# Kernel optimization log

Hardware: AMD Instinct MI355X
Metric: run time of the kernel (lower is better)

## Reference

```python
import jax, jax.numpy as jnp
import numpy as np

RANK = 16
RATIO_1 = 0.01
RATIO_2 = 0.01
N_POWER_ITERS = 2  # randomized SVD power iterations (torch.svd_lowrank-style)


def _lowrank_V(A, rank, key):
    """Randomized low-rank right factor V (n, rank) of A (m, n), a la svd_lowrank."""
    m, n = A.shape
    omega = jax.random.normal(key, (n, rank), dtype=A.dtype)
    Q, _ = jnp.linalg.qr(A @ omega)              # (m, rank)
    for _ in range(N_POWER_ITERS):
        Z, _ = jnp.linalg.qr(A.T @ Q)            # (n, rank)
        Q, _ = jnp.linalg.qr(A @ Z)              # (m, rank)
    B = Q.T @ A                                  # (rank, n) small
    _, _, Vt = jnp.linalg.svd(B, full_matrices=False)
    return Vt.T                                  # (n, rank), orthonormal cols


def _get_statistics(x, ratio):
    # threshold such that ~ratio fraction of |x| entries are outliers
    return jnp.quantile(jnp.abs(x), 1.0 - ratio)


def _compress(x, thresh, rank, key):
    d = x.shape[-1]
    x2d = x.reshape(-1, d)                       # (M, D)
    outliers = jnp.where(jnp.abs(x2d) > thresh, x2d, jnp.zeros((), x2d.dtype))
    residual = x2d - outliers
    R = _lowrank_V(residual, rank, key)          # (D, rank)
    L = residual @ R                             # (M, rank)
    Rinv = R.T                                   # orthonormal cols -> pinv = R^T
    return outliers, L, R, Rinv


def reference(x1, x2):
    # Hadamard product (the module's returned value)
    result = x1 * x2
    # iteration == 0 path: compute statistics and run SVD compression
    out1 = _get_statistics(x1, RATIO_1)
    out2 = _get_statistics(x2, RATIO_2)
    k = jax.random.key(42)
    k1, k2 = jax.random.split(k)
    _, _, R1, Rinv1 = _compress(x1, out1, RANK, k1)
    _, _, R2, Rinv2 = _compress(x2, out2, RANK, k2)
    return (result, out1, R1, Rinv1, out2, R2, Rinv2)


def setup_inputs() -> dict:
    key = jax.random.key(0)
    k1, k2 = jax.random.split(key)
    x1 = jax.random.normal(k1, (4, 2048, 4096), dtype=jnp.float32)
    x2 = jax.random.normal(k2, (4, 2048, 4096), dtype=jnp.float32)
    return {"x1": x1, "x2": x2}
```

## Files before the change

### kernel.cpp

```cpp
#include <hip/hip_runtime.h>
#include <cstdint>
#include <cstddef>


#define DEV __device__ __forceinline__

typedef float nfloat4 __attribute__((ext_vector_type(4)));

constexpr long long NTOT = 33554432LL;
constexpr unsigned long long KSEL = 33218888ULL;

constexpr long long OUT_T1  = 33554432LL;
constexpr long long OUT_R1  = 33554433LL;
constexpr long long OUT_RI1 = 33619969LL;
constexpr long long OUT_T2  = 33685505LL;
constexpr long long OUT_R2  = 33685506LL;
constexpr long long OUT_RI2 = 33751042LL;

constexpr size_t OFF_SPEC   = 0;
constexpr size_t OFF_BPART  = 0;
constexpr size_t OFF_FB     = 4194304;
constexpr size_t OFF_CNT    = 6291456;
constexpr size_t ZERO_FLOATS= 6291472;
constexpr size_t OFF_CHIST  = 6291456;
constexpr size_t OFF_COARSE = 8388608;
constexpr size_t OFF_SEGS   = 8392704;
constexpr size_t OFF_SELR   = 8394752;
constexpr size_t OFF_TSEL   = 8394768;
constexpr size_t OFF_OMT    = 8394784;
constexpr size_t OFF_BIGY   = 8525856;
constexpr size_t OFF_BIGQ   = 8788000;
constexpr size_t OFF_ZT     = 9050144;
constexpr size_t OFF_QQR    = 9181216;
constexpr size_t OFF_TMAT   = 9312288;
constexpr size_t OFF_GRAMP  = 9443360;
constexpr size_t OFF_S      = 9476128;
constexpr size_t OFF_QTOP   = 9476640;
constexpr size_t OFF_RG     = 9477152;
constexpr size_t OFF_VTL    = 9477664;

#define TFR(a,b,r) { a += b; b = (b << r) | (b >> (32 - r)); b ^= a; }

DEV void d_threefry(uint32_t k0, uint32_t k1, uint32_t x0, uint32_t x1,
                    uint32_t& o0, uint32_t& o1){
  uint32_t ks2 = k0 ^ k1 ^ 0x1BD11BDAu;
  x0 += k0; x1 += k1;
  TFR(x0,x1,13) TFR(x0,x1,15) TFR(x0,x1,26) TFR(x0,x1,6)
  x0 += k1; x1 += ks2 + 1u;
  TFR(x0,x1,17) TFR(x0,x1,29) TFR(x0,x1,16) TFR(x0,x1,24)
  x0 += ks2; x1 += k0 + 2u;
  TFR(x0,x1,13) TFR(x0,x1,15) TFR(x0,x1,26) TFR(x0,x1,6)
  x0 += k0; x1 += k1 + 3u;
  TFR(x0,x1,17) TFR(x0,x1,29) TFR(x0,x1,16) TFR(x0,x1,24)
  x0 += k1; x1 += ks2 + 4u;
  TFR(x0,x1,13) TFR(x0,x1,15) TFR(x0,x1,26) TFR(x0,x1,6)
  x0 += ks2; x1 += k0 + 5u;
  o0 = x0; o1 = x1;
}

static void h_threefry(uint32_t k0, uint32_t k1, uint32_t x0, uint32_t x1,
                       uint32_t& o0, uint32_t& o1){
  uint32_t ks2 = k0 ^ k1 ^ 0x1BD11BDAu;
  x0 += k0; x1 += k1;
  TFR(x0,x1,13) TFR(x0,x1,15) TFR(x0,x1,26) TFR(x0,x1,6)
  x0 += k1; x1 += ks2 + 1u;
  TFR(x0,x1,17) TFR(x0,x1,29) TFR(x0,x1,16) TFR(x0,x1,24)
  x0 += ks2; x1 += k0 + 2u;
  TFR(x0,x1,13) TFR(x0,x1,15) TFR(x0,x1,26) TFR(x0,x1,6)
  x0 += k0; x1 += k1 + 3u;
  TFR(x0,x1,17) TFR(x0,x1,29) TFR(x0,x1,16) TFR(x0,x1,24)
  x0 += k1; x1 += ks2 + 4u;
  TFR(x0,x1,13) TFR(x0,x1,15) TFR(x0,x1,26) TFR(x0,x1,6)
  x0 += ks2; x1 += k0 + 5u;
  o0 = x0; o1 = x1;
}

DEV float erfinv_f32(float x){
  float w = -log1pf(-x*x);
  float p;
  if (w < 5.0f){
    w -= 2.5f;
    p = 2.81022636e-08f;
    p = fmaf(p, w, 3.43273939e-07f);
    p = fmaf(p, w, -3.5233877e-06f);
    p = fmaf(p, w, -4.39150654e-06f);
    p = fmaf(p, w, 0.00021858087f);
    p = fmaf(p, w, -0.00125372503f);
    p = fmaf(p, w, -0.00417768164f);
    p = fmaf(p, w, 0.246640727f);
    p = fmaf(p, w, 1.50140941f);
  } else {
    w = sqrtf(w) - 3.0f;
    p = -0.000200214257f;
    p = fmaf(p, w, 0.000100950558f);
    p = fmaf(p, w, 0.00134934322f);
    p = fmaf(p, w, -0.00367342844f);
    p = fmaf(p, w, 0.00573950773f);
    p = fmaf(p, w, -0.0076224613f);
    p = fmaf(p, w, 0.00943887047f);
    p = fmaf(p, w, 1.00167406f);
    p = fmaf(p, w, 2.83297682f);
  }
  return p * x;
}

DEV float lapy2f(float x, float y){
  float xa = fabsf(x), ya = fabsf(y);
  float w = fmaxf(xa, ya), z = fminf(xa, ya);
  if (z == 0.f) return w;
  float q = z / w;
  return w * sqrtf(1.f + q*q);
}

DEV void slartg_(float f, float g, float& c, float& s, float& r){
  if (g == 0.f){ c = 1.f; s = 0.f; r = f; }
  else if (f == 0.f){ c = 0.f; s = copysignf(1.f, g); r = fabsf(g); }
  else {
    float d = sqrtf(f*f + g*g);
    c = fabsf(f) / d;
    r = copysignf(d, f);
    s = g / r;
  }
}

DEV void slas2_(float f, float g, float h, float& ssmin, float& ssmax){
  float fa = fabsf(f), ga = fabsf(g), ha = fabsf(h);
  float fhmn = fminf(fa, ha), fhmx = fmaxf(fa, ha);
  if (fhmn == 0.f){
    ssmin = 0.f;
    if (fhmx == 0.f) ssmax = ga;
    else {
      float mx = fmaxf(fhmx, ga), mn = fminf(fhmx, ga);
      float q = mn/mx;
      ssmax = mx*sqrtf(1.f + q*q);
    }
  } else {
    if (ga < fhmx){
      float as_ = 1.f + fhmn/fhmx;
      float at_ = (fhmx - fhmn)/fhmx;
      float au = ga/fhmx; au = au*au;
      float cc = 2.f/(sqrtf(as_*as_ + au) + sqrtf(at_*at_ + au));
      ssmin = fhmn*cc; ssmax = fhmx/cc;
    } else {
      float au = fhmx/ga;
      if (au == 0.f){ ssmin = (fhmn*fhmx)/ga; ssmax = ga; }
      else {
        float as_ = 1.f + fhmn/fhmx;
        float at_ = (fhmx - fhmn)/fhmx;
        float q1 = as_*au, q2 = at_*au;
        float cc = 1.f/(sqrtf(1.f + q1*q1) + sqrtf(1.f + q2*q2));
        ssmin = (fhmn*cc)*au; ssmin = ssmin + ssmin;
        ssmax = ga/(cc + cc);
      }
    }
  }
}

DEV void slasv2_(float f, float g, float h, float& ssmin, float& ssmax,
                 float& snr, float& csr, float& snl, float& csl){
  const float eps = 5.9604645e-08f;
  float ft = f, fa = fabsf(f), ht = h, ha = fabsf(h);
  int pmax = 1;
  bool swp = (ha > fa);
  if (swp){ pmax = 3; float t; t=ft; ft=ht; ht=t; t=fa; fa=ha; ha=t; }
  float gt = g, ga = fabsf(g);
  float clt = 0.f, crt = 0.f, slt = 0.f, srt = 0.f;
  if (ga == 0.f){ ssmin = ha; ssmax = fa; clt = 1.f; crt = 1.f; slt = 0.f; srt = 0.f; }
  else {
    bool gasmal = true;
    if (ga > fa){
      pmax = 2;
      if ((fa/ga) < eps){
        gasmal = false;
        ssmax = ga;
        if (ha > 1.f) ssmin = fa/(ga/ha); else ssmin = (fa/ga)*ha;
        clt = 1.f; slt = ht/gt; srt = 1.f; crt = ft/gt;
      }
    }
    if (gasmal){
      float dd = fa - ha;
      float L = (dd == fa) ? 1.f : dd/fa;
      float Mv = gt/ft;
      float T = 2.f - L;
      float MM = Mv*Mv, TT = T*T;
      float Sv = sqrtf(TT + MM);
      float Rv = (L == 0.f) ? fabsf(Mv) : sqrtf(L*L + MM);
      float Av = 0.5f*(Sv + Rv);
      ssmin = ha/Av; ssmax = fa*Av;
      float Tv;
      if (MM == 0.f){
        if (L == 0.f) Tv = copysignf(2.f, ft)*copysignf(1.f, gt);
        else Tv = gt/copysignf(dd, ft) + Mv/T;
      } else {
        Tv = (Mv/(Sv + T) + Mv/(Rv + L))*(1.f + Av);
      }
      float Lv = sqrtf(Tv*Tv + 4.f);
      crt = 2.f/Lv; srt = Tv/Lv;
      clt = (crt + srt*Mv)/Av;
      slt = (ht/ft)*srt/Av;
    }
  }
  if (swp){ csl = srt; snl = crt; csr = slt; snr = clt; }
  else    { csl = clt; snl = slt; csr = crt; snr = srt; }
  float tsign = 1.f;
  if (pmax == 1) tsign = copysignf(1.f, csr)*copysignf(1.f, csl)*copysignf(1.f, f);
  if (pmax == 2) tsign = copysignf(1.f, snr)*copysignf(1.f, csl)*copysignf(1.f, g);
  if (pmax == 3) tsign = copysignf(1.f, snr)*copysignf(1.f, snl)*copysignf(1.f, h);
  ssmax = copysignf(ssmax, tsign);
  ssmin = copysignf(ssmin, tsign*copysignf(1.f, f)*copysignf(1.f, h));
}

__global__ __launch_bounds__(256) void k_had(const float* __restrict__ x1,
    const float* __restrict__ x2, float* __restrict__ out, float* __restrict__ ws){
  uint32_t* cnt = (uint32_t*)(ws + OFF_CNT);
  uint32_t* s1 = (uint32_t*)(ws + OFF_SPEC);
  uint32_t* s2 = s1 + 2097152;
  const float4* a4 = (const float4*)x1;
  const float4* b4 = (const float4*)x2;
  nfloat4* o4 = (nfloat4*)out;
  int cb1 = 0, c11 = 0, c21 = 0, cb2 = 0, c12 = 0, c22 = 0;
  long long n4 = NTOT/4;
  long long stride = (long long)gridDim.x * 256;
  for (long long i = (long long)blockIdx.x*256 + threadIdx.x; i < n4; i += stride){
    float4 a = a4[i], b = b4[i];
    nfloat4 o;
    o.x = a.x*b.x; o.y = a.y*b.y; o.z = a.z*b.z; o.w = a.w*b.w;
    __builtin_nontemporal_store(o, &o4[i]);
    uint32_t u, dd;
    u = __float_as_uint(a.x)&0x7fffffffu; cb1 += (u < 0x40100000u);
    dd = u - 0x40100000u;
    if (dd < 0x200000u){ atomicAdd(&s1[dd], 1u); if (dd < 0x100000u) c11++; else c21++; }
    u = __float_as_uint(a.y)&0x7fffffffu; cb1 += (u < 0x40100000u);
    dd = u - 0x40100000u;
    if (dd < 0x200000u){ atomicAdd(&s1[dd], 1u); if (dd < 0x100000u) c11++; else c21++; }
    u = __float_as_uint(a.z)&0x7fffffffu; cb1 += (u < 0x40100000u);
    dd = u - 0x40100000u;
    if (dd < 0x200000u){ atomicAdd(&s1[dd], 1u); if (dd < 0x100000u) c11++; else c21++; }
    u = __float_as_uint(a.w)&0x7fffffffu; cb1 += (u < 0x40100000u);
    dd = u - 0x40100000u;
    if (dd < 0x200000u){ atomicAdd(&s1[dd], 1u); if (dd < 0x100000u) c11++; else c21++; }
    u = __float_as_uint(b.x)&0x7fffffffu; cb2 += (u < 0x40100000u);
    dd = u - 0x40100000u;
    if (dd < 0x200000u){ atomicAdd(&s2[dd], 1u); if (dd < 0x100000u) c12++; else c22++; }
    u = __float_as_uint(b.y)&0x7fffffffu; cb2 += (u < 0x40100000u);
    dd = u - 0x40100000u;
    if (dd < 0x200000u){ atomicAdd(&s2[dd], 1u); if (dd < 0x100000u) c12++; else c22++; }
    u = __float_as_uint(b.z)&0x7fffffffu; cb2 += (u < 0x40100000u);
    dd = u - 0x40100000u;
    if (dd < 0x200000u){ atomicAdd(&s2[dd], 1u); if (dd < 0x100000u) c12++; else c22++; }
    u = __float_as_uint(b.w)&0x7fffffffu; cb2 += (u < 0x40100000u);
    dd = u - 0x40100000u;
    if (dd < 0x200000u){ atomicAdd(&s2[dd], 1u); if (dd < 0x100000u) c12++; else c22++; }
  }
  #pragma unroll
  for (int off = 32; off > 0; off >>= 1){
    cb1 += __shfl_xor(cb1, off, 64);
    c11 += __shfl_xor(c11, off, 64);
    c21 += __shfl_xor(c21, off, 64);
    cb2 += __shfl_xor(cb2, off, 64);
    c12 += __shfl_xor(c12, off, 64);
    c22 += __shfl_xor(c22, off, 64);
  }
  if ((threadIdx.x & 63) == 0){
    atomicAdd(&cnt[0], (uint32_t)cb1);
    atomicAdd(&cnt[1], (uint32_t)c11);
    atomicAdd(&cnt[2], (uint32_t)c21);
    atomicAdd(&cnt[3], (uint32_t)cb2);
    atomicAdd(&cnt[4], (uint32_t)c12);
    atomicAdd(&cnt[5], (uint32_t)c22);
  }
}

__global__ __launch_bounds__(64) void k_select(float* __restrict__ ws){
  if (threadIdx.x != 0) return;
  int ty = blockIdx.x;
  const uint32_t* cnt = (const uint32_t*)(ws + OFF_CNT) + ty*3;
  int* selr = (int*)(ws + OFF_SELR) + ty*4;
  unsigned long long cb = cnt[0], c1 = cnt[1], c2 = cnt[2], K = KSEL;
  if (K >= cb && K < cb + c1){
    selr[0] = 0x401; selr[1] = (int)(K - cb); selr[2] = 1;
  } else if (K >= cb + c1 && K < cb + c1 + c2){
    selr[0] = 0x402; selr[1] = (int)(K - cb - c1); selr[2] = 1;
  } else {
    selr[2] = 0;
  }
}

__global__ __launch_bounds__(256) void k_hist_fb(const float* __restrict__ x1,
    const float* __restrict__ x2, float* __restrict__ ws){
  const int* selr = (const int*)(ws + OFF_SELR);
  if (selr[2] && selr[4 + 2]) return;
  __shared__ uint32_t lh[2][4][2048];
  for (int i = threadIdx.x; i < 2*4*2048; i += 256) (&lh[0][0][0])[i] = 0u;
  __syncthreads();
  int rep = threadIdx.x & 3;
  const float4* a4 = (const float4*)x1;
  const float4* b4 = (const float4*)x2;
  long long n4 = NTOT/4;
  long long stride = (long long)gridDim.x * 256;
  for (long long i = (long long)blockIdx.x*256 + threadIdx.x; i < n4; i += stride){
    float4 a = a4[i], b = b4[i];
    uint32_t u;
    u = __float_as_uint(a.x)&0x7fffffffu; atomicAdd(&lh[0][rep][u>>20], 1u);
    u = __float_as_uint(a.y)&0x7fffffffu; atomicAdd(&lh[0][rep][u>>20], 1u);
    u = __float_as_uint(a.z)&0x7fffffffu; atomicAdd(&lh[0][rep][u>>20], 1u);
    u = __float_as_uint(a.w)&0x7fffffffu; atomicAdd(&lh[0][rep][u>>20], 1u);
    u = __float_as_uint(b.x)&0x7fffffffu; atomicAdd(&lh[1][rep][u>>20], 1u);
    u = __float_as_uint(b.y)&0x7fffffffu; atomicAdd(&lh[1][rep][u>>20], 1u);
    u = __float_as_uint(b.z)&0x7fffffffu; atomicAdd(&lh[1][rep][u>>20], 1u);
    u = __float_as_uint(b.w)&0x7fffffffu; atomicAdd(&lh[1][rep][u>>20], 1u);
  }
  __syncthreads();
  uint32_t* ch = (uint32_t*)(ws + OFF_CHIST);
  for (int i = threadIdx.x; i < 2048; i += 256){
    uint32_t c0 = lh[0][0][i] + lh[0][1][i] + lh[0][2][i] + lh[0][3][i];
    uint32_t c1 = lh[1][0][i] + lh[1][1][i] + lh[1][2][i] + lh[1][3][i];
    ch[((size_t)blockIdx.x*2 + 0)*2048 + i] = c0;
    ch[((size_t)blockIdx.x*2 + 1)*2048 + i] = c1;
  }
}

__global__ __launch_bounds__(256) void k_coarse_red(float* __restrict__ ws){
  int ty = blockIdx.y;
  if (((const int*)(ws + OFF_SELR))[ty*4 + 2]) return;
  const uint32_t* ch = (const uint32_t*)(ws + OFF_CHIST);
  uint32_t* h = (uint32_t*)(ws + OFF_COARSE) + ty*2048;
  int bin = blockIdx.x*128 + (threadIdx.x & 127);
  int half = threadIdx.x >> 7;
  uint32_t s = 0;
  for (int p = half*256; p < half*256 + 256; p++)
    s += ch[((size_t)p*2 + ty)*2048 + bin];
  __shared__ uint32_t sh[256];
  sh[threadIdx.x] = s;
  __syncthreads();
  if (threadIdx.x < 128) h[bin] = sh[threadIdx.x] + sh[threadIdx.x + 128];
}

__global__ __launch_bounds__(256) void k_coarse_scan(float* __restrict__ ws){
  int ty = blockIdx.x;
  int* selr = (int*)(ws + OFF_SELR) + ty*4;
  if (selr[2]) return;
  const uint32_t* h = (const uint32_t*)(ws + OFF_COARSE) + ty*2048;
  __shared__ unsigned long long ps[256];
  unsigned long long s = 0;
  for (int j = 0; j < 8; j++) s += h[threadIdx.x*8 + j];
  ps[threadIdx.x] = s;
  __syncthreads();
  if (threadIdx.x == 0){
    unsigned long long cum = 0, K = KSEL;
    int g = 0;
    for (; g < 256; g++){ if (cum + ps[g] > K) break; cum += ps[g]; }
    if (g > 255) g = 255;
    int bin = 2047;
    for (int j = 0; j < 8; j++){
      uint32_t c = h[g*8 + j];
      if (cum + c > K){ bin = g*8 + j; break; }
      cum += c;
    }
    selr[0] = bin;
    selr[1] = (int)(K - cum);
    selr[2] = 0;
  }
}

__global__ __launch_bounds__(256) void k_fine_fb(const float* __restrict__ x1,
    const float* __restrict__ x2, float* __restrict__ ws){
  int ty = blockIdx.y;
  const int* selr = (const int*)(ws + OFF_SELR) + ty*4;
  if (selr[2]) return;
  const float4* x4 = (const float4*)(ty ? x2 : x1);
  uint32_t bin = (uint32_t)selr[0];
  uint32_t* f = (uint32_t*)(ws + OFF_FB) + ((size_t)ty<<20);
  long long n4 = NTOT/4;
  long long stride = (long long)gridDim.x * 256;
  for (long long i = (long long)blockIdx.x*256 + threadIdx.x; i < n4; i += stride){
    float4 a = x4[i];
    uint32_t u;
    u = __float_as_uint(a.x)&0x7fffffffu; if ((u>>20)==bin) atomicAdd(&f[u&0xFFFFFu],1u);
    u = __float_as_uint(a.y)&0x7fffffffu; if ((u>>20)==bin) atomicAdd(&f[u&0xFFFFFu],1u);
    u = __float_as_uint(a.z)&0x7fffffffu; if ((u>>20)==bin) atomicAdd(&f[u&0xFFFFFu],1u);
    u = __float_as_uint(a.w)&0x7fffffffu; if ((u>>20)==bin) atomicAdd(&f[u&0xFFFFFu],1u);
  }
}

DEV const uint32_t* fine_base(const float* ws, int ty){
  const int* selr = (const int*)(ws + OFF_SELR) + ty*4;
  if (selr[2])
    return (const uint32_t*)(ws + OFF_SPEC) + ((size_t)ty<<21)
           + (((uint32_t)selr[0] - 0x401u) << 20);
  return (const uint32_t*)(ws + OFF_FB) + ((size_t)ty<<20);
}

__global__ __launch_bounds__(256) void k_seg_sum(float* __restrict__ ws){
  int ty = blockIdx.y;
  const uint32_t* f = fine_base(ws, ty);
  uint32_t* segs = (uint32_t*)(ws + OFF_SEGS) + ty*1024;
  uint32_t s = 0;
  int base = blockIdx.x*1024;
  for (int k = 0; k < 4; k++) s += f[base + k*256 + threadIdx.x];
  __shared__ uint32_t sh[256];
  sh[threadIdx.x] = s;
  __syncthreads();
  for (int off = 128; off > 0; off >>= 1){
    if (threadIdx.x < off) sh[threadIdx.x] += sh[threadIdx.x + off];
    __syncthreads();
  }
  if (threadIdx.x == 0) segs[blockIdx.x] = sh[0];
}

__global__ __launch_bounds__(256) void k_fine_scan2(float* __restrict__ ws, float* __restrict__ out){
  int ty = blockIdx.x;
  const uint32_t* f = fine_base(ws, ty);
  const uint32_t* segs = (const uint32_t*)(ws + OFF_SEGS) + ty*1024;
  const int* selr = (const int*)(ws + OFF_SELR) + ty*4;
  __shared__ uint32_t sh[1024];
  __shared__ uint32_t ps[256];
  __shared__ int gsel; __shared__ uint32_t csel;
  int t = threadIdx.x;
  uint32_t K = (uint32_t)selr[1];
  for (int k = 0; k < 4; k++) sh[k*256 + t] = segs[k*256 + t];
  __syncthreads();
  ps[t] = sh[4*t] + sh[4*t+1] + sh[4*t+2] + sh[4*t+3];
  __syncthreads();
  if (t == 0){
    uint32_t cum = 0; int q = 0;
    for (; q < 256; q++){ if (cum + ps[q] > K) break; cum += ps[q]; }
    if (q > 255) q = 255;
    int g = q*4;
    for (int j = 0; j < 4; j++){
      uint32_t c = sh[q*4 + j];
      if (cum + c > K){ g = q*4 + j; break; }
      cum += c;
      if (j == 3) g = q*4 + 3;
    }
    gsel = g; csel = cum;
  }
  __syncthreads();
  int g = gsel;
  for (int k = 0; k < 4; k++) sh[k*256 + t] = f[(size_t)g*1024 + k*256 + t];
  __syncthreads();
  ps[t] = sh[4*t] + sh[4*t+1] + sh[4*t+2] + sh[4*t+3];
  __syncthreads();
  if (t == 0){
    uint32_t cum = csel; int q = 0;
    for (; q < 256; q++){ if (cum + ps[q] > K) break; cum += ps[q]; }
    if (q > 255) q = 255;
    int j = q*4 + 3;
    for (int jj = 0; jj < 4; jj++){
      uint32_t c = sh[q*4 + jj];
      if (cum + c > K){ j = q*4 + jj; break; }
      cum += c;
    }
    uint32_t bits = (((uint32_t)selr[0])<<20) | (uint32_t)((g*1024 + j) & 0xFFFFF);
    float th = __uint_as_float(bits);
    ws[OFF_TSEL + ty] = th;
    out[ty ? OUT_T2 : OUT_T1] = th;
  }
}

__global__ __launch_bounds__(256) void k_omega(uint32_t a0, uint32_t a1,
    uint32_t b0, uint32_t b1, float* __restrict__ ws){
  int ty = blockIdx.y;
  uint32_t k0 = ty ? b0 : a0, k1 = ty ? b1 : a1;
  int i = blockIdx.x*256 + threadIdx.x;
  uint32_t o0, o1;
  d_threefry(k0, k1, 0u, (uint32_t)i, o0, o1);
  uint32_t bits = o0 ^ o1;
  float fr = __uint_as_float((bits >> 9) | 0x3f800000u) - 1.0f;
  const float lo = -0.99999994f;
  float u = fr * 2.0f + lo;
  u = fmaxf(lo, u);
  float v = 1.41421356237f * erfinv_f32(u);
  int row = i >> 4, col = i & 15;
  ws[OFF_OMT + (size_t)ty*65536 + (size_t)col*4096 + row] = v;
}

__global__ __launch_bounds__(256) void k_atype(const float* __restrict__ x1,
    const float* __restrict__ x2, float* __restrict__ ws, size_t wtOff){
  int ty = blockIdx.y;
  const float* x = ty ? x2 : x1;
  const float* wt = ws + wtOff + (size_t)ty*65536;
  float* Y = ws + OFF_BIGY + (size_t)ty*131072;
  float t = ws[OFF_TSEL + ty];
  int wave = threadIdx.x >> 6, lane = threadIdx.x & 63;
  __shared__ __align__(16) float wts[16][256];
  __shared__ float outs[16][16];
  float acc[4][16];
  #pragma unroll
  for (int r = 0; r < 4; r++)
    #pragma unroll
    for (int j = 0; j < 16; j++) acc[r][j] = 0.f;
  int rowbase = blockIdx.x*16 + wave*4;
  for (int c = 0; c < 4096; c += 256){
    __syncthreads();
    for (int idx = threadIdx.x; idx < 16*64; idx += 256){
      int j = idx >> 6, q = idx & 63;
      ((float4*)&wts[j][0])[q] = ((const float4*)(wt + (size_t)j*4096 + c))[q];
    }
    __syncthreads();
    float4 xv[4];
    #pragma unroll
    for (int rr = 0; rr < 4; rr++){
      int row = rowbase + rr;
      float4 a = ((const float4*)(x + (size_t)row*4096 + c))[lane];
      a.x = fabsf(a.x) > t ? 0.f : a.x;
      a.y = fabsf(a.y) > t ? 0.f : a.y;
      a.z = fabsf(a.z) > t ? 0.f : a.z;
      a.w = fabsf(a.w) > t ? 0.f : a.w;
      xv[rr] = a;
    }
    #pragma unroll
    for (int j = 0; j < 16; j++){
      float4 w4 = ((const float4*)&wts[j][0])[lane];
      #pragma unroll
      for (int rr = 0; rr < 4; rr++){
        acc[rr][j] = fmaf(xv[rr].x, w4.x, acc[rr][j]);
        acc[rr][j] = fmaf(xv[rr].y, w4.y, acc[rr][j]);
        acc[rr][j] = fmaf(xv[rr].z, w4.z, acc[rr][j]);
        acc[rr][j] = fmaf(xv[rr].w, w4.w, acc[rr][j]);
      }
    }
  }
  #pragma unroll
  for (int rr = 0; rr < 4; rr++)
    for (int j = 0; j < 16; j++){
      float v = acc[rr][j];
      for (int off = 32; off > 0; off >>= 1) v += __shfl_xor(v, off, 64);
      if (lane == 0) outs[wave*4 + rr][j] = v;
    }
  __syncthreads();
  int r = threadIdx.x >> 4, cc = threadIdx.x & 15;
  Y[(size_t)(blockIdx.x*16 + r)*16 + cc] = outs[r][cc];
}

__global__ __launch_bounds__(256) void k_gramP(float* __restrict__ ws, size_t mOff,
    size_t mStr){
  int ty = blockIdx.y;
  const float* M = ws + mOff + (size_t)ty*mStr;
  float* gp = ws + OFF_GRAMP + (size_t)(ty*64 + blockIdx.x)*256;
  __shared__ __align__(16) float buf[128][16];
  int t = threadIdx.x;
  for (int q = t; q < 512; q += 256)
    ((float4*)&buf[0][0])[q] = ((const float4*)(M + (size_t)blockIdx.x*2048))[q];
  __syncthreads();
  int i = t >> 4, j = t & 15;
  float s = 0.f;
  int rstart = (blockIdx.x == 0) ? 16 : 0;
  for (int r = rstart; r < 128; r++) s += buf[r][i]*buf[r][j];
  gp[t] = s;
}

__global__ __launch_bounds__(256) void k_btype(const float* __restrict__ x1,
    const float* __restrict__ x2, float* __restrict__ ws){
  int ty = blockIdx.y;
  const float* x = ty ? x2 : x1;
  const float* Q = ws + OFF_BIGQ + (size_t)ty*131072;
  float t = ws[OFF_TSEL + ty];
  int cb = blockIdx.x & 15;
  int rc = blockIdx.x >> 4;
  int c = cb*256 + threadIdx.x;
  int r0 = rc*512;
  __shared__ __align__(16) float Qs[64][16];
  float acc[16];
  #pragma unroll
  for (int j = 0; j < 16; j++) acc[j] = 0.f;
  for (int tile = 0; tile < 8; tile++){
    __syncthreads();
    ((float4*)&Qs[0][0])[threadIdx.x] =
        ((const float4*)(Q + (size_t)(r0 + tile*64)*16))[threadIdx.x];
    __syncthreads();
    const float* xp = x + (size_t)(r0 + tile*64)*4096 + c;
    #pragma unroll 4
    for (int rr = 0; rr < 64; rr++){
      float v = xp[(size_t)rr*4096];
      v = fabsf(v) > t ? 0.f : v;
      float4 qa = ((const float4*)&Qs[rr][0])[0];
      float4 qb = ((const float4*)&Qs[rr][0])[1];
      float4 qc = ((const float4*)&Qs[rr][0])[2];
      float4 qd = ((const float4*)&Qs[rr][0])[3];
      acc[ 0] = fmaf(v, qa.x, acc[ 0]);
      acc[ 1] = fmaf(v, qa.y, acc[ 1]);
      acc[ 2] = fmaf(v, qa.z, acc[ 2]);
      acc[ 3] = fmaf(v, qa.w, acc[ 3]);
      acc[ 4] = fmaf(v, qb.x, acc[ 4]);
      acc[ 5] = fmaf(v, qb.y, acc[ 5]);
      acc[ 6] = fmaf(v, qb.z, acc[ 6]);
      acc[ 7] = fmaf(v, qb.w, acc[ 7]);
      acc[ 8] = fmaf(v, qc.x, acc[ 8]);
      acc[ 9] = fmaf(v, qc.y, acc[ 9]);
      acc[10] = fmaf(v, qc.z, acc[10]);
      acc[11] = fmaf(v, qc.w, acc[11]);
      acc[12] = fmaf(v, qd.x, acc[12]);
      acc[13] = fmaf(v, qd.y, acc[13]);
      acc[14] = fmaf(v, qd.z, acc[14]);
      acc[15] = fmaf(v, qd.w, acc[15]);
    }
  }
  float* BP = ws + OFF_BPART + (((size_t)(ty*16 + rc))<<16) + (size_t)c*16;
  #pragma unroll
  for (int q = 0; q < 4; q++){
    float4 o; o.x = acc[q*4]; o.y = acc[q*4+1]; o.z = acc[q*4+2]; o.w = acc[q*4+3];
    ((float4*)BP)[q] = o;
  }
}

__global__ __launch_bounds__(256) void k_bredgram(float* __restrict__ ws){
  int ty = blockIdx.y;
  const float* BP = ws + OFF_BPART + (((size_t)ty*16)<<16);
  float* T = ws + OFF_TMAT + (size_t)ty*65536;
  float* gp = ws + OFF_GRAMP + (size_t)(ty*64 + blockIdx.x)*256;
  __shared__ float sh[64][16];
  int t = threadIdx.x;
  for (int k = 0; k < 4; k++){
    int e = blockIdx.x*1024 + k*256 + t;
    float s = 0.f;
    #pragma unroll
    for (int rc = 0; rc < 16; rc++) s += BP[((size_t)rc<<16) + e];
    T[e] = s;
    int le = k*256 + t;
    sh[le >> 4][le & 15] = s;
  }
  __syncthreads();
  int i = t >> 4, j = t & 15;
  float s = 0.f;
  int rstart = (blockIdx.x == 0) ? 16 : 0;
  for (int r = rstart; r < 64; r++) s += sh[r][i]*sh[r][j];
  gp[t] = s;
}

__global__ __launch_bounds__(64) void k_tiny(float* __restrict__ ws, size_t mOff,
    size_t mStr){
  int ty = blockIdx.x;
  const float* Mp = ws + mOff + (size_t)ty*mStr;
  float* sOut = ws + OFF_S + ty*256;
  float* qtOut = ws + OFF_QTOP + ty*256;
  float* rgOut = ws + OFF_RG + ty*256;
  __shared__ float G[16][16];
  __shared__ float Cld[32][16];
  __shared__ float bc[4];
  __shared__ float tau[16];
  int l = threadIdx.x;
  int j = l & 15;
  for (int e = l; e < 256; e += 64){
    const float* gp = ws + OFF_GRAMP + (size_t)ty*16384 + e;
    float s = 0.f;
    for (int p = 0; p < 64; p++) s += gp[(size_t)p*256];
    G[e>>4][e&15] = s;
  }
  for (int idx = l; idx < 256; idx += 64)
    Cld[idx>>4][idx&15] = Mp[idx];
  __syncthreads();
  for (int k = 0; k < 16; k++){
    float dk = sqrtf(G[k][k]);
    if (l == k) G[k][k] = dk;
    else if (l > k && l < 16) G[k][l] = G[k][l] / dk;
    __syncthreads();
    if (l > k && l < 16)
      for (int jj = l; jj < 16; jj++) G[l][jj] -= G[k][l]*G[k][jj];
    __syncthreads();
  }
  float Cc[32];
  #pragma unroll
  for (int r = 0; r < 32; r++){
    if (r < 16) Cc[r] = Cld[r][j];
    else Cc[r] = (j >= r - 16) ? G[r-16][j] : 0.f;
  }
  #pragma unroll
  for (int i = 0; i < 16; i++){
    if (l == i){
      float alpha = Cc[i];
      float ssum = 0.f;
      #pragma unroll
      for (int r = i+1; r < 32; r++) ssum += Cc[r]*Cc[r];
      float xn = sqrtf(ssum);
      float beta, tv, sc;
      if (xn == 0.f){ tv = 0.f; beta = alpha; sc = 1.f; }
      else {
        beta = -copysignf(lapy2f(alpha, xn), alpha);
        tv = (beta - alpha)/beta;
        sc = 1.f/(alpha - beta);
        #pragma unroll
        for (int r = i+1; r < 32; r++) Cc[r] *= sc;
      }
      Cc[i] = beta;
      bc[0] = beta; bc[1] = tv;
      tau[i] = tv;
      #pragma unroll
      for (int r = i; r < 32; r++) Cld[r][i] = Cc[r];
    }
    __syncthreads();
    float tv = bc[1];
    if (tv != 0.f && l < 16 && j > i){
      float w = Cc[i];
      #pragma unroll
      for (int r = i+1; r < 32; r++) w += Cld[r][i]*Cc[r];
      w *= tv;
      Cc[i] -= w;
      #pragma unroll
      for (int r = i+1; r < 32; r++) Cc[r] -= w*Cld[r][i];
    }
    __syncthreads();
  }
  float Qc[32];
  #pragma unroll
  for (int r = 0; r < 32; r++) Qc[r] = 0.f;
  #pragma unroll
  for (int i = 15; i >= 0; i--){
    float tv = tau[i];
    if (i < 15 && l < 16 && j > i){
      float w = Qc[i];
      #pragma unroll
      for (int r = i+1; r < 32; r++) w += Cld[r][i]*Qc[r];
      w *= tv;
      Qc[i] -= w;
      #pragma unroll
      for (int r = i+1; r < 32; r++) Qc[r] -= w*Cld[r][i];
    }
// ... 144 lines not shown
  for (int k = 0; k < 16; k++){
    D[k] = d_[k];
    E[k] = (k < 15) ? e_[k] : 0.f;
    vt[k] = (k == l) ? 1.f : 0.f;
  }
  auto getD = [&](int i)->float{ float r = D[0];
    #pragma unroll
    for (int k = 1; k < 16; k++) if (i == k) r = D[k];
    return r; };
  auto setD = [&](int i, float v){
    #pragma unroll
    for (int k = 0; k < 16; k++) if (i == k) D[k] = v; };
  auto getE = [&](int i)->float{ float r = E[0];
    #pragma unroll
    for (int k = 1; k < 16; k++) if (i == k) r = E[k];
    return r; };
  auto setE = [&](int i, float v){
    #pragma unroll
    for (int k = 0; k < 16; k++) if (i == k) E[k] = v; };
  auto getVt = [&](int i)->float{ float r = vt[0];
    #pragma unroll
    for (int k = 1; k < 16; k++) if (i == k) r = vt[k];
    return r; };
  auto setVt = [&](int i, float v){
    #pragma unroll
    for (int k = 0; k < 16; k++) if (i == k) vt[k] = v; };

  const float eps = 5.9604645e-08f;
  const float unfl = 1.17549435e-38f;
  const float tol = 10.f*eps;
  float sminoa = fabsf(D[0]);
  if (sminoa != 0.f){
    float mu = sminoa;
    #pragma unroll
    for (int i = 1; i < 16; i++){
      mu = fabsf(D[i])*(mu/(mu + fabsf(E[i-1])));
      sminoa = fminf(sminoa, mu);
    }
  }
  sminoa = sminoa / sqrtf((float)n);
  float thresh = fmaxf(tol*sminoa, (float)(6*n*n)*unfl);
  int maxit = 6*n*n;
  int iter = 0, oldll = -1, oldm = -1, mm = n, idir = 0;
  while (true){
    if (mm <= 1) break;
    if (iter > maxit) break;
    float smaxw = fabsf(getD(mm-1));
    int llv = 1; bool split = false;
    {
      bool done = false;
      #pragma unroll
      for (int c = 14; c >= 0; c--){
        if (c <= mm-2 && !done){
          if (fabsf(E[c]) <= thresh){ split = true; llv = c+1; done = true; }
          else smaxw = fmaxf(smaxw, fmaxf(fabsf(D[c]), fabsf(E[c])));
        }
      }
    }
    if (split){
      setE(llv-1, 0.f);
      if (llv == mm-1){ mm = mm - 1; continue; }
      llv = llv + 1;
    }
    if (llv == mm-1){
      float sigmn, sigmx, sinr, cosr, sinl, cosl;
      slasv2_(getD(mm-2), getE(mm-2), getD(mm-1), sigmn, sigmx, sinr, cosr, sinl, cosl);
      setD(mm-2, sigmx); setE(mm-2, 0.f); setD(mm-1, sigmn);
      float t1 = getVt(mm-2), t2 = getVt(mm-1);
      setVt(mm-2, cosr*t1 + sinr*t2);
      setVt(mm-1, cosr*t2 - sinr*t1);
      mm -= 2;
      continue;
    }
    if (llv > oldm || mm < oldll)
      idir = (fabsf(getD(llv-1)) >= fabsf(getD(mm-1))) ? 1 : 2;
    bool deflated = false;
    float sminl = 0.f;
    if (idir == 1){
      if (fabsf(getE(mm-2)) <= tol*fabsf(getD(mm-1))){ setE(mm-2, 0.f); continue; }
      float mu = fabsf(getD(llv-1)); sminl = mu;
      #pragma unroll
      for (int c = 0; c < 15; c++){
        if (c >= llv-1 && c <= mm-2 && !deflated){
          if (fabsf(E[c]) <= tol*mu){ E[c] = 0.f; deflated = true; }
          else {
            mu = fabsf(D[c+1])*(mu/(mu + fabsf(E[c])));
            sminl = fminf(sminl, mu);
          }
        }
      }
    } else {
      if (fabsf(getE(llv-1)) <= tol*fabsf(getD(llv-1))){ setE(llv-1, 0.f); continue; }
      float mu = fabsf(getD(mm-1)); sminl = mu;
      #pragma unroll
      for (int c = 14; c >= 0; c--){
        if (c >= llv-1 && c <= mm-2 && !deflated){
          if (fabsf(E[c]) <= tol*mu){ E[c] = 0.f; deflated = true; }
          else {
            mu = fabsf(D[c])*(mu/(mu + fabsf(E[c])));
            sminl = fminf(sminl, mu);
          }
        }
      }
    }
    if (deflated) continue;
    oldll = llv; oldm = mm;
    float shift = 0.f, rdum;
    if (!((float)n*tol*(sminl/smaxw) <= fmaxf(eps, 0.01f*tol))){
      float sll;
      if (idir == 1){ sll = fabsf(getD(llv-1)); slas2_(getD(mm-2), getE(mm-2), getD(mm-1), shift, rdum); }
      else          { sll = fabsf(getD(mm-1));  slas2_(getD(llv-1), getE(llv-1), getD(llv), shift, rdum); }
      if (sll > 0.f){ float q = shift/sll; if (q*q < eps) shift = 0.f; }
    }
    iter += mm - llv;
    if (shift == 0.f){
      if (idir == 1){
        float cs = 1.f, oldcs = 1.f, sn = 0.f, oldsn = 0.f, rr, dnew;
        #pragma unroll
        for (int i0 = 0; i0 < 15; i0++){
          if (i0 >= llv-1 && i0 <= mm-2){
            slartg_(D[i0]*cs, E[i0], cs, sn, rr);
            if (i0 > llv-1) E[i0-1 < 0 ? 0 : i0-1] = oldsn*rr;
            slartg_(oldcs*rr, D[i0+1]*sn, oldcs, oldsn, dnew);
            D[i0] = dnew;
            if (cs != 1.f || sn != 0.f){
              float t1 = vt[i0], t2 = vt[i0+1];
              vt[i0+1] = cs*t2 - sn*t1;
              vt[i0]   = sn*t2 + cs*t1;
            }
          }
        }
        float h = getD(mm-1)*cs;
        setD(mm-1, h*oldcs);
        float hv = h*oldsn;
        setE(mm-2, (fabsf(hv) <= thresh) ? 0.f : hv);
      } else {
        float cs = 1.f, oldcs = 1.f, sn = 0.f, oldsn = 0.f, rr, dnew;
        #pragma unroll
        for (int i0 = 15; i0 >= 1; i0--){
          if (i0 >= llv && i0 <= mm-1){
            slartg_(D[i0]*cs, E[i0-1], cs, sn, rr);
            if (i0 < mm-1) E[i0] = oldsn*rr;
            slartg_(oldcs*rr, D[i0-1]*sn, oldcs, oldsn, dnew);
            D[i0] = dnew;
            float cR = oldcs, sR = -oldsn;
            if (cR != 1.f || sR != 0.f){
              float t1 = vt[i0-1], t2 = vt[i0];
              vt[i0]   = cR*t2 - sR*t1;
              vt[i0-1] = sR*t2 + cR*t1;
            }
          }
        }
        float h = getD(llv-1)*cs;
        setD(llv-1, h*oldcs);
        float hv = h*oldsn;
        setE(llv-1, (fabsf(hv) <= thresh) ? 0.f : hv);
      }
    } else {
      if (idir == 1){
        float dl = getD(llv-1);
        float ff = (fabsf(dl) - shift)*(copysignf(1.f, dl) + shift/dl);
        float gg = getE(llv-1);
        float cosr, sinr, cosl, sinl, rr;
        #pragma unroll
        for (int i0 = 0; i0 < 15; i0++){
          if (i0 >= llv-1 && i0 <= mm-2){
            slartg_(ff, gg, cosr, sinr, rr);
            if (i0 > llv-1) E[i0-1 < 0 ? 0 : i0-1] = rr;
            float di = D[i0], ei = E[i0];
            ff = cosr*di + sinr*ei;
            E[i0] = cosr*ei - sinr*di;
            gg = sinr*D[i0+1];
            D[i0+1] = cosr*D[i0+1];
            slartg_(ff, gg, cosl, sinl, rr);
            D[i0] = rr;
            float ei2 = E[i0], dip = D[i0+1];
            ff = cosl*ei2 + sinl*dip;
            D[i0+1] = cosl*dip - sinl*ei2;
            if (i0 < mm-2){
              gg = sinl*E[i0+1];
              E[i0+1] = cosl*E[i0+1];
            }
            if (cosr != 1.f || sinr != 0.f){
              float t1 = vt[i0], t2 = vt[i0+1];
              vt[i0+1] = cosr*t2 - sinr*t1;
              vt[i0]   = sinr*t2 + cosr*t1;
            }
          }
        }
        setE(mm-2, (fabsf(ff) <= thresh) ? 0.f : ff);
      } else {
        float dm = getD(mm-1);
        float ff = (fabsf(dm) - shift)*(copysignf(1.f, dm) + shift/dm);
        float gg = getE(mm-2);
        float cosr, sinr, cosl, sinl, rr;
        #pragma unroll
        for (int i0 = 15; i0 >= 1; i0--){
          if (i0 >= llv && i0 <= mm-1){
            slartg_(ff, gg, cosr, sinr, rr);
            if (i0 < mm-1) E[i0] = rr;
            float di = D[i0], eim = E[i0-1];
            ff = cosr*di + sinr*eim;
            E[i0-1] = cosr*eim - sinr*di;
            gg = sinr*D[i0-1];
            D[i0-1] = cosr*D[i0-1];
            slartg_(ff, gg, cosl, sinl, rr);
            D[i0] = rr;
            float eim2 = E[i0-1], dim = D[i0-1];
            ff = cosl*eim2 + sinl*dim;
            D[i0-1] = cosl*dim - sinl*eim2;
            if (i0 > llv){
              gg = sinl*E[i0-2 < 0 ? 0 : i0-2];
              E[i0-2 < 0 ? 0 : i0-2] = cosl*E[i0-2 < 0 ? 0 : i0-2];
            }
            float cR = cosr, sR = -sinr;
            if (cR != 1.f || sR != 0.f){
              float t1 = vt[i0-1], t2 = vt[i0];
              vt[i0]   = cR*t2 - sR*t1;
              vt[i0-1] = sR*t2 + cR*t1;
            }
          }
        }
        setE(llv-1, (fabsf(ff) <= thresh) ? 0.f : ff);
      }
    }
  }
  #pragma unroll
  for (int k = 0; k < 16; k++){
    if (D[k] < 0.f){ D[k] = -D[k]; vt[k] = -vt[k]; }
  }
  #pragma unroll
  for (int i = 1; i <= 15; i++){
    int isub = 1; float smn = D[0];
    #pragma unroll
    for (int jj = 2; jj <= 16; jj++){
      if (jj <= 16 + 1 - i){
        if (D[jj-1] <= smn){ isub = jj; smn = D[jj-1]; }
      }
    }
    if (isub != 16 + 1 - i){
      setD(isub - 1, D[16 - i]);
      D[16 - i] = smn;
      float tmp = getVt(isub - 1);
      setVt(isub - 1, vt[16 - i]);
      vt[16 - i] = tmp;
    }
  }
  if (l < 16){
    #pragma unroll
    for (int r = 0; r < 16; r++) VTm[r][l] = vt[r];
  }
  __syncthreads();
  for (int i = n-2; i >= 0; i--){
    float tp = taup[i];
    if (tp != 0.f && l < 16){
      int r = l;
      float w = VTm[r][i+1];
      for (int c = i+2; c < n; c++) w += VTm[r][c]*A[i][c];
      w *= tp;
      VTm[r][i+1] -= w;
      for (int c = i+2; c < n; c++) VTm[r][c] -= w*A[i][c];
    }
    __syncthreads();
  }
  for (int idx = l; idx < 256; idx += 64) vtlOut[idx] = VTm[idx>>4][idx&15];
}

__global__ __launch_bounds__(256) void k_rout(float* __restrict__ ws, float* __restrict__ out){
  int ty = blockIdx.y;
  const float* Qq = ws + OFF_QQR + (size_t)ty*65536;
  const float* vtl = ws + OFF_VTL + ty*256;
  long long Roff  = ty ? OUT_R2  : OUT_R1;
  long long RIoff = ty ? OUT_RI2 : OUT_RI1;
  __shared__ float V[16][16];
  int t = threadIdx.x;
  V[t>>4][t&15] = vtl[t];
  __syncthreads();
  int row = blockIdx.x*256 + t;
  float mv[16];
  #pragma unroll
  for (int q = 0; q < 4; q++){
    float4 v = ((const float4*)(Qq + (size_t)row*16))[q];
    mv[q*4] = v.x; mv[q*4+1] = v.y; mv[q*4+2] = v.z; mv[q*4+3] = v.w;
  }
  #pragma unroll
  for (int j = 0; j < 16; j++){
    float s = 0.f;
    #pragma unroll
    for (int i = 0; i < 16; i++) s = fmaf(mv[i], V[j][i], s);
    out[Roff + (long long)row*16 + j] = s;
    out[RIoff + (long long)j*4096 + row] = s;
  }
}

extern "C" void kernel_launch(void* const* d_in, const int* in_sizes, int n_in,
                              void* d_out, int out_size, void* d_ws, size_t ws_size,
                              hipStream_t stream){
  const float* x1 = (const float*)d_in[0];
  const float* x2 = (const float*)d_in[1];
  float* out = (float*)d_out;
  float* ws = (float*)d_ws;
  (void)in_sizes; (void)n_in; (void)out_size; (void)ws_size;

  hipMemsetAsync(d_ws, 0, ZERO_FLOATS*sizeof(float), stream);

  k_had<<<dim3(1024), 256, 0, stream>>>(x1, x2, out, ws);
  k_select<<<dim3(2), 64, 0, stream>>>(ws);
  k_hist_fb<<<dim3(512), 256, 0, stream>>>(x1, x2, ws);
  k_coarse_red<<<dim3(16, 2), 256, 0, stream>>>(ws);
  k_coarse_scan<<<dim3(2), 256, 0, stream>>>(ws);
  k_fine_fb<<<dim3(1024, 2), 256, 0, stream>>>(x1, x2, ws);
  k_seg_sum<<<dim3(1024, 2), 256, 0, stream>>>(ws);
  k_fine_scan2<<<dim3(2), 256, 0, stream>>>(ws, out);

  uint32_t a0, a1, b0, b1;
  h_threefry(0u, 42u, 0u, 0u, a0, a1);
  h_threefry(0u, 42u, 0u, 1u, b0, b1);
  k_omega<<<dim3(256, 2), 256, 0, stream>>>(a0, a1, b0, b1, ws);

  k_atype<<<dim3(512, 2), 256, 0, stream>>>(x1, x2, ws, OFF_OMT);
  k_gramP<<<dim3(64, 2), 256, 0, stream>>>(ws, OFF_BIGY, 131072);
  k_tiny<<<dim3(2), 64, 0, stream>>>(ws, OFF_BIGY, 131072);
  k_applyq<<<dim3(32, 2), 256, 0, stream>>>(ws, OFF_BIGY, 131072, OFF_BIGQ, 131072, 8192, 1, 0);
  k_btype<<<dim3(256, 2), 256, 0, stream>>>(x1, x2, ws);
  k_bredgram<<<dim3(64, 2), 256, 0, stream>>>(ws);
  k_tiny<<<dim3(2), 64, 0, stream>>>(ws, OFF_TMAT, 65536);
  k_applyq<<<dim3(16, 2), 256, 0, stream>>>(ws, OFF_TMAT, 65536, OFF_ZT, 65536, 4096, 0, 1);
  k_atype<<<dim3(512, 2), 256, 0, stream>>>(x1, x2, ws, OFF_ZT);
  k_gramP<<<dim3(64, 2), 256, 0, stream>>>(ws, OFF_BIGY, 131072);
  k_tiny<<<dim3(2), 64, 0, stream>>>(ws, OFF_BIGY, 131072);
  k_applyq<<<dim3(32, 2), 256, 0, stream>>>(ws, OFF_BIGY, 131072, OFF_BIGQ, 131072, 8192, 1, 0);
  k_btype<<<dim3(256, 2), 256, 0, stream>>>(x1, x2, ws);
  k_bredgram<<<dim3(64, 2), 256, 0, stream>>>(ws);
  k_tiny<<<dim3(2), 64, 0, stream>>>(ws, OFF_TMAT, 65536);
  k_applyq<<<dim3(16, 2), 256, 0, stream>>>(ws, OFF_TMAT, 65536, OFF_ZT, 65536, 4096, 0, 1);
  k_atype<<<dim3(512, 2), 256, 0, stream>>>(x1, x2, ws, OFF_ZT);
  k_gramP<<<dim3(64, 2), 256, 0, stream>>>(ws, OFF_BIGY, 131072);
  k_tiny<<<dim3(2), 64, 0, stream>>>(ws, OFF_BIGY, 131072);
  k_applyq<<<dim3(32, 2), 256, 0, stream>>>(ws, OFF_BIGY, 131072, OFF_BIGQ, 131072, 8192, 1, 0);
  k_btype<<<dim3(256, 2), 256, 0, stream>>>(x1, x2, ws);
  k_bredgram<<<dim3(64, 2), 256, 0, stream>>>(ws);
  k_tiny<<<dim3(2), 64, 0, stream>>>(ws, OFF_TMAT, 65536);
  k_applyq<<<dim3(16, 2), 256, 0, stream>>>(ws, OFF_TMAT, 65536, OFF_QQR, 65536, 4096, 1, 0);

  k_chain<<<dim3(2), 64, 0, stream>>>(ws);
  k_rout<<<dim3(16, 2), 256, 0, stream>>>(ws, out);
}
```

Baseline: 1.854 ms.

## Replace global speculative fine histogram with per-block shared-memory two-level select

The Hadamard pass now builds a coarse 2048-bin histogram of the speculative window in shared memory and writes one partial per block, instead of doing global atomics into a 2M-entry speculative histogram. New kernels reduce the partials, select a coarse bin, rescan the input with shared-memory atomics to build a 1024-bin fine histogram, and pick the threshold. The memset shrinks because the large speculative region no longer needs zeroing. The cost is an extra full read of each input for the fine pass and 16MB of per-block partials to write and reduce.

Measured after the change: 1.705 ms. 1.09x faster.

```diff
diff --git a/kernel.cpp b/kernel.cpp
--- a/kernel.cpp
+++ b/kernel.cpp
@@ -9,6 +9,7 @@
 
 constexpr long long NTOT = 33554432LL;
 constexpr unsigned long long KSEL = 33218888ULL;
+constexpr uint32_t WLO = 0x40100000u;
 
 constexpr long long OUT_T1  = 33554432LL;
 constexpr long long OUT_R1  = 33554433LL;
@@ -17,11 +18,13 @@
 constexpr long long OUT_R2  = 33685506LL;
 constexpr long long OUT_RI2 = 33751042LL;
 
-constexpr size_t OFF_SPEC   = 0;
+constexpr size_t OFF_WPART  = 0;
 constexpr size_t OFF_BPART  = 0;
 constexpr size_t OFF_FB     = 4194304;
 constexpr size_t OFF_CNT    = 6291456;
-constexpr size_t ZERO_FLOATS= 6291472;
+constexpr size_t OFF_GF     = 6291472;
+constexpr size_t ZERO_BASE  = OFF_FB;
+constexpr size_t ZERO_FLOATS= 2099216;
 constexpr size_t OFF_CHIST  = 6291456;
 constexpr size_t OFF_COARSE = 8388608;
 constexpr size_t OFF_SEGS   = 8392704;
@@ -212,13 +215,14 @@
 
 __global__ __launch_bounds__(256) void k_had(const float* __restrict__ x1,
     const float* __restrict__ x2, float* __restrict__ out, float* __restrict__ ws){
+  __shared__ uint32_t wh[2][2048];
+  for (int i = threadIdx.x; i < 4096; i += 256) (&wh[0][0])[i] = 0u;
+  __syncthreads();
   uint32_t* cnt = (uint32_t*)(ws + OFF_CNT);
-  uint32_t* s1 = (uint32_t*)(ws + OFF_SPEC);
-  uint32_t* s2 = s1 + 2097152;
   const float4* a4 = (const float4*)x1;
   const float4* b4 = (const float4*)x2;
   nfloat4* o4 = (nfloat4*)out;
-  int cb1 = 0, c11 = 0, c21 = 0, cb2 = 0, c12 = 0, c22 = 0;
+  uint32_t cb1 = 0, cb2 = 0;
   long long n4 = NTOT/4;
   long long stride = (long long)gridDim.x * 256;
   for (long long i = (long long)blockIdx.x*256 + threadIdx.x; i < n4; i += stride){
@@ -227,62 +231,141 @@
     o.x = a.x*b.x; o.y = a.y*b.y; o.z = a.z*b.z; o.w = a.w*b.w;
     __builtin_nontemporal_store(o, &o4[i]);
     uint32_t u, dd;
-    u = __float_as_uint(a.x)&0x7fffffffu; cb1 += (u < 0x40100000u);
-    dd = u - 0x40100000u;
-    if (dd < 0x200000u){ atomicAdd(&s1[dd], 1u); if (dd < 0x100000u) c11++; else c21++; }
-    u = __float_as_uint(a.y)&0x7fffffffu; cb1 += (u < 0x40100000u);
-    dd = u - 0x40100000u;
-    if (dd < 0x200000u){ atomicAdd(&s1[dd], 1u); if (dd < 0x100000u) c11++; else c21++; }
-    u = __float_as_uint(a.z)&0x7fffffffu; cb1 += (u < 0x40100000u);
-    dd = u - 0x40100000u;
-    if (dd < 0x200000u){ atomicAdd(&s1[dd], 1u); if (dd < 0x100000u) c11++; else c21++; }
-    u = __float_as_uint(a.w)&0x7fffffffu; cb1 += (u < 0x40100000u);
-    dd = u - 0x40100000u;
-    if (dd < 0x200000u){ atomicAdd(&s1[dd], 1u); if (dd < 0x100000u) c11++; else c21++; }
-    u = __float_as_uint(b.x)&0x7fffffffu; cb2 += (u < 0x40100000u);
-    dd = u - 0x40100000u;
-    if (dd < 0x200000u){ atomicAdd(&s2[dd], 1u); if (dd < 0x100000u) c12++; else c22++; }
-    u = __float_as_uint(b.y)&0x7fffffffu; cb2 += (u < 0x40100000u);
-    dd = u - 0x40100000u;
-    if (dd < 0x200000u){ atomicAdd(&s2[dd], 1u); if (dd < 0x100000u) c12++; else c22++; }
-    u = __float_as_uint(b.z)&0x7fffffffu; cb2 += (u < 0x40100000u);
-    dd = u - 0x40100000u;
-    if (dd < 0x200000u){ atomicAdd(&s2[dd], 1u); if (dd < 0x100000u) c12++; else c22++; }
-    u = __float_as_uint(b.w)&0x7fffffffu; cb2 += (u < 0x40100000u);
-    dd = u - 0x40100000u;
-    if (dd < 0x200000u){ atomicAdd(&s2[dd], 1u); if (dd < 0x100000u) c12++; else c22++; }
-  }
+    u = __float_as_uint(a.x)&0x7fffffffu; cb1 += (u < WLO); dd = u - WLO;
+    if (dd < 0x200000u) atomicAdd(&wh[0][dd>>10], 1u);
+    u = __float_as_uint(a.y)&0x7fffffffu; cb1 += (u < WLO); dd = u - WLO;
+    if (dd < 0x200000u) atomicAdd(&wh[0][dd>>10], 1u);
+    u = __float_as_uint(a.z)&0x7fffffffu; cb1 += (u < WLO); dd = u - WLO;
+    if (dd < 0x200000u) atomicAdd(&wh[0][dd>>10], 1u);
+    u = __float_as_uint(a.w)&0x7fffffffu; cb1 += (u < WLO); dd = u - WLO;
+    if (dd < 0x200000u) atomicAdd(&wh[0][dd>>10], 1u);
+    u = __float_as_uint(b.x)&0x7fffffffu; cb2 += (u < WLO); dd = u - WLO;
+    if (dd < 0x200000u) atomicAdd(&wh[1][dd>>10], 1u);
+    u = __float_as_uint(b.y)&0x7fffffffu; cb2 += (u < WLO); dd = u - WLO;
+    if (dd < 0x200000u) atomicAdd(&wh[1][dd>>10], 1u);
+    u = __float_as_uint(b.z)&0x7fffffffu; cb2 += (u < WLO); dd = u - WLO;
+    if (dd < 0x200000u) atomicAdd(&wh[1][dd>>10], 1u);
+    u = __float_as_uint(b.w)&0x7fffffffu; cb2 += (u < WLO); dd = u - WLO;
+    if (dd < 0x200000u) atomicAdd(&wh[1][dd>>10], 1u);
+  }
+  __syncthreads();
+  uint32_t* wp = (uint32_t*)(ws + OFF_WPART) + (size_t)blockIdx.x*4096;
+  for (int i = threadIdx.x; i < 4096; i += 256) wp[i] = (&wh[0][0])[i];
   #pragma unroll
   for (int off = 32; off > 0; off >>= 1){
     cb1 += __shfl_xor(cb1, off, 64);
-    c11 += __shfl_xor(c11, off, 64);
-    c21 += __shfl_xor(c21, off, 64);
     cb2 += __shfl_xor(cb2, off, 64);
-    c12 += __shfl_xor(c12, off, 64);
-    c22 += __shfl_xor(c22, off, 64);
   }
   if ((threadIdx.x & 63) == 0){
-    atomicAdd(&cnt[0], (uint32_t)cb1);
-    atomicAdd(&cnt[1], (uint32_t)c11);
-    atomicAdd(&cnt[2], (uint32_t)c21);
-    atomicAdd(&cnt[3], (uint32_t)cb2);
-    atomicAdd(&cnt[4], (uint32_t)c12);
-    atomicAdd(&cnt[5], (uint32_t)c22);
-  }
-}
-
-__global__ __launch_bounds__(64) void k_select(float* __restrict__ ws){
-  if (threadIdx.x != 0) return;
+    atomicAdd(&cnt[0], cb1);
+    atomicAdd(&cnt[1], cb2);
+  }
+}
+
+__global__ __launch_bounds__(1024) void k_red(float* __restrict__ ws){
+  int ty = blockIdx.y;
+  const uint32_t* wp = (const uint32_t*)(ws + OFF_WPART);
+  uint32_t* H = (uint32_t*)(ws + OFF_COARSE) + ty*2048;
+  int t = threadIdx.x;
+  int bin = blockIdx.x*256 + (t & 255);
+  int pq = t >> 8;
+  uint32_t s = 0;
+  for (int p = pq*256; p < pq*256 + 256; p++)
+    s += wp[(size_t)p*4096 + (size_t)ty*2048 + bin];
+  __shared__ uint32_t sh[1024];
+  sh[t] = s;
+  __syncthreads();
+  if (t < 256) H[bin] = sh[t] + sh[t+256] + sh[t+512] + sh[t+768];
+}
+
+__global__ __launch_bounds__(256) void k_wselect(float* __restrict__ ws){
   int ty = blockIdx.x;
-  const uint32_t* cnt = (const uint32_t*)(ws + OFF_CNT) + ty*3;
+  const uint32_t* H = (const uint32_t*)(ws + OFF_COARSE) + ty*2048;
+  const uint32_t* cnt = (const uint32_t*)(ws + OFF_CNT);
   int* selr = (int*)(ws + OFF_SELR) + ty*4;
-  unsigned long long cb = cnt[0], c1 = cnt[1], c2 = cnt[2], K = KSEL;
-  if (K >= cb && K < cb + c1){
-    selr[0] = 0x401; selr[1] = (int)(K - cb); selr[2] = 1;
-  } else if (K >= cb + c1 && K < cb + c1 + c2){
-    selr[0] = 0x402; selr[1] = (int)(K - cb - c1); selr[2] = 1;
-  } else {
-    selr[2] = 0;
+  __shared__ unsigned long long ps[256];
+  unsigned long long s = 0;
+  for (int j = 0; j < 8; j++) s += H[threadIdx.x*8 + j];
+  ps[threadIdx.x] = s;
+  __syncthreads();
+  if (threadIdx.x == 0){
+    unsigned long long K = KSEL, cum = cnt[ty];
+    int valid = 0, sbin = 0, rank = 0;
+    if (K >= cum){
+      int g = 0;
+      for (; g < 256; g++){ if (cum + ps[g] > K) break; cum += ps[g]; }
+      if (g < 256){
+        for (int j = 0; j < 8; j++){
+          uint32_t c = H[g*8 + j];
+          if (cum + c > K){ sbin = g*8 + j; rank = (int)(K - cum); valid = 1; break; }
+          cum += c;
+        }
+      }
+    }
+    selr[0] = sbin; selr[1] = rank; selr[2] = valid;
+  }
+}
+
+__global__ __launch_bounds__(256) void k_fine(const float* __restrict__ x1,
+    const float* __restrict__ x2, float* __restrict__ ws){
+  int ty = blockIdx.y;
+  const int* selr = (const int*)(ws + OFF_SELR) + ty*4;
+  if (!selr[2]) return;
+  uint32_t g = (uint32_t)selr[0];
+  __shared__ uint32_t lh[1024];
+  for (int i = threadIdx.x; i < 1024; i += 256) lh[i] = 0u;
+  __syncthreads();
+  const float4* x4 = (const float4*)(ty ? x2 : x1);
+  long long n4 = NTOT/4;
+  long long stride = (long long)gridDim.x * 256;
+  for (long long i = (long long)blockIdx.x*256 + threadIdx.x; i < n4; i += stride){
+    float4 a = x4[i];
+    uint32_t dd;
+    dd = (__float_as_uint(a.x)&0x7fffffffu) - WLO;
+    if ((dd>>10) == g) atomicAdd(&lh[dd & 1023u], 1u);
+    dd = (__float_as_uint(a.y)&0x7fffffffu) - WLO;
+    if ((dd>>10) == g) atomicAdd(&lh[dd & 1023u], 1u);
+    dd = (__float_as_uint(a.z)&0x7fffffffu) - WLO;
+    if ((dd>>10) == g) atomicAdd(&lh[dd & 1023u], 1u);
+    dd = (__float_as_uint(a.w)&0x7fffffffu) - WLO;
+    if ((dd>>10) == g) atomicAdd(&lh[dd & 1023u], 1u);
+  }
+  __syncthreads();
+  uint32_t* gf = (uint32_t*)(ws + OFF_GF) + (size_t)ty*1024;
+  for (int i = threadIdx.x; i < 1024; i += 256){
+    uint32_t v = lh[i];
+    if (v) atomicAdd(&gf[i], v);
+  }
+}
+
+__global__ __launch_bounds__(256) void k_fine_sel(float* __restrict__ ws,
+    float* __restrict__ out){
+  int ty = blockIdx.x;
+  const int* selr = (const int*)(ws + OFF_SELR) + ty*4;
+  if (!selr[2]) return;
+  const uint32_t* gf = (const uint32_t*)(ws + OFF_GF) + (size_t)ty*1024;
+  __shared__ uint32_t sh[1024];
+  __shared__ uint32_t ps[256];
+  int t = threadIdx.x;
+  for (int k = 0; k < 4; k++) sh[k*256 + t] = gf[k*256 + t];
+  __syncthreads();
+  ps[t] = sh[4*t] + sh[4*t+1] + sh[4*t+2] + sh[4*t+3];
+  __syncthreads();
+  if (t == 0){
+    uint32_t K = (uint32_t)selr[1];
+    uint32_t cum = 0; int q = 0;
+    for (; q < 256; q++){ if (cum + ps[q] > K) break; cum += ps[q]; }
+    if (q > 255) q = 255;
+    int f = q*4 + 3;
+    for (int jj = 0; jj < 4; jj++){
+      uint32_t c = sh[q*4 + jj];
+      if (cum + c > K){ f = q*4 + jj; break; }
+      cum += c;
+    }
+    uint32_t bits = WLO + (((uint32_t)selr[0]) << 10) + (uint32_t)f;
+    float th = __uint_as_float(bits);
+    ws[OFF_TSEL + ty] = th;
+    out[ty ? OUT_T2 : OUT_T1] = th;
   }
 }
 
@@ -359,7 +442,6 @@
     }
     selr[0] = bin;
     selr[1] = (int)(K - cum);
-    selr[2] = 0;
   }
 }
 
@@ -383,17 +465,11 @@
   }
 }
 
-DEV const uint32_t* fine_base(const float* ws, int ty){
-  const int* selr = (const int*)(ws + OFF_SELR) + ty*4;
-  if (selr[2])
-    return (const uint32_t*)(ws + OFF_SPEC) + ((size_t)ty<<21)
-           + (((uint32_t)selr[0] - 0x401u) << 20);
-  return (const uint32_t*)(ws + OFF_FB) + ((size_t)ty<<20);
-}
-
 __global__ __launch_bounds__(256) void k_seg_sum(float* __restrict__ ws){
   int ty = blockIdx.y;
-  const uint32_t* f = fine_base(ws, ty);
+  const int* selr = (const int*)(ws + OFF_SELR) + ty*4;
+  if (selr[2]) return;
+  const uint32_t* f = (const uint32_t*)(ws + OFF_FB) + ((size_t)ty<<20);
   uint32_t* segs = (uint32_t*)(ws + OFF_SEGS) + ty*1024;
   uint32_t s = 0;
   int base = blockIdx.x*1024;
@@ -410,9 +486,10 @@
 
 __global__ __launch_bounds__(256) void k_fine_scan2(float* __restrict__ ws, float* __restrict__ out){
   int ty = blockIdx.x;
-  const uint32_t* f = fine_base(ws, ty);
+  const int* selr = (const int*)(ws + OFF_SELR) + ty*4;
+  if (selr[2]) return;
+  const uint32_t* f = (const uint32_t*)(ws + OFF_FB) + ((size_t)ty<<20);
   const uint32_t* segs = (const uint32_t*)(ws + OFF_SEGS) + ty*1024;
-  const int* selr = (const int*)(ws + OFF_SELR) + ty*4;
   __shared__ uint32_t sh[1024];
   __shared__ uint32_t ps[256];
   __shared__ int gsel; __shared__ uint32_t csel;
@@ -1163,10 +1240,13 @@
   float* ws = (float*)d_ws;
   (void)in_sizes; (void)n_in; (void)out_size; (void)ws_size;
 
-  hipMemsetAsync(d_ws, 0, ZERO_FLOATS*sizeof(float), stream);
+  hipMemsetAsync(ws + ZERO_BASE, 0, ZERO_FLOATS*sizeof(float), stream);
 
   k_had<<<dim3(1024), 256, 0, stream>>>(x1, x2, out, ws);
-  k_select<<<dim3(2), 64, 0, stream>>>(ws);
+  k_red<<<dim3(8, 2), 1024, 0, stream>>>(ws);
+  k_wselect<<<dim3(2), 256, 0, stream>>>(ws);
+  k_fine<<<dim3(1024, 2), 256, 0, stream>>>(x1, x2, ws);
+  k_fine_sel<<<dim3(2), 256, 0, stream>>>(ws, out);
   k_hist_fb<<<dim3(512), 256, 0, stream>>>(x1, x2, ws);
   k_coarse_red<<<dim3(16, 2), 256, 0, stream>>>(ws);
   k_coarse_scan<<<dim3(2), 256, 0, stream>>>(ws);
```
